# Performance work log

Hardware: AMD Instinct MI355X
Metric: run time of the kernel (lower is better)

Reference implementation:

```python
import jax, jax.numpy as jnp
import numpy as np

B, D_IN, D_H = 16384, 512, 1024


def _glorot(key, out_d, in_d):
    lim = 1.0 / np.sqrt(in_d)
    return jax.random.uniform(key, (out_d, in_d), minval=-lim, maxval=lim, dtype=jnp.float32)


def setup_inputs() -> dict:
    key = jax.random.key(0)
    ks = jax.random.split(key, 16)
    inp = {
        "x_t": jax.random.normal(ks[0], (B, D_IN), dtype=jnp.float32),
        "delta_t": jax.random.uniform(ks[1], (B, 1), dtype=jnp.float32),
        "h_prev": jax.random.normal(ks[2], (B, D_H), dtype=jnp.float32),
        # torch nn.Linear weights are [out, in]; y = x @ W.T
        "W_sh": _glorot(ks[3], D_H, D_H),
        "W_sx": _glorot(ks[4], D_H, D_IN),
        "W_st": _glorot(ks[5], D_H, 1),
        "b_s": jnp.zeros((D_H,), jnp.float32),
        "WTh": _glorot(ks[6], D_H, D_H),
        "WTx": _glorot(ks[7], D_H, D_IN),
        "WTs": _glorot(ks[8], D_H, D_H),
        "b_T": jnp.zeros((D_H,), jnp.float32),
        "W_rh": _glorot(ks[9], D_H, D_H),
        "W_rx": _glorot(ks[10], D_H, D_IN),
        "b_r": jnp.zeros((D_H,), jnp.float32),
        "W_zh": _glorot(ks[11], D_H, D_H),
        "W_zx": _glorot(ks[12], D_H, D_IN),
        "b_z": jnp.zeros((D_H,), jnp.float32),
        "W_h": _glorot(ks[13], D_H, D_H),
        "W_x": _glorot(ks[14], D_H, D_IN),
        "b": jnp.zeros((D_H,), jnp.float32),
    }
    return inp


def reference(x_t, delta_t, h_prev,
              W_sh, W_sx, W_st, b_s,
              WTh, WTx, WTs, b_T,
              W_rh, W_rx, b_r,
              W_zh, W_zx, b_z,
              W_h, W_x, b):
    lin = lambda x, W: x @ W.T  # nn.Linear(bias=False)
    s_t = jnp.tanh(lin(h_prev, W_sh) + lin(x_t, W_sx) + lin(delta_t, W_st) + b_s)
    T_t = jax.nn.sigmoid(lin(h_prev, WTh) + lin(x_t, WTx) + lin(s_t, WTs) + b_T)
    r_t = jax.nn.sigmoid(lin(h_prev, W_rh) + lin(x_t, W_rx) + b_r)
    z_t = jax.nn.sigmoid(lin(h_prev, W_zh) + lin(x_t, W_zx) + b_z)
    h_tilde = jnp.tanh(lin(r_t * h_prev, W_h) + lin(x_t, W_x) + b)
    h_t = (1.0 - z_t) * (T_t * h_prev) + z_t * h_tilde
    return h_t
```

## Files before the change

kernel.cpp:

```cpp
#include <hip/hip_runtime.h>
#include <stdint.h>

#define AS1 __attribute__((address_space(1)))
#define AS3 __attribute__((address_space(3)))

typedef unsigned short US;
typedef __bf16 bf16x8 __attribute__((ext_vector_type(8)));
typedef float f32x4 __attribute__((ext_vector_type(4)));
typedef int intx4 __attribute__((ext_vector_type(4)));

static constexpr int Bsz = 16384;
static constexpr int DIN = 512;
static constexpr int DH  = 1024;
static constexpr int LDA = 2560;
static constexpr int LDR = 1536;

__device__ __forceinline__ US f2bf(float f) {
  unsigned u = __float_as_uint(f);
  u += 0x7fffu + ((u >> 16) & 1u);
  return (US)(u >> 16);
}
__device__ __forceinline__ float bf2f(US u) { return __uint_as_float(((unsigned)u) << 16); }
__device__ __forceinline__ float sigm(float x) { return 1.f / (1.f + __expf(-x)); }
__device__ __forceinline__ float tanh_f(float x) { return 1.f - 2.f / (1.f + __expf(2.f * x)); }

__device__ __forceinline__ intx4 dsr128(unsigned addr) {
  intx4 r;
  asm volatile("ds_read_b128 %0, %1" : "=v"(r) : "v"(addr));
  return r;
}

#define BARR  __builtin_amdgcn_s_barrier()
#define SB0   __builtin_amdgcn_sched_barrier(0)
#define LGKM0 { asm volatile("s_waitcnt lgkmcnt(0)"); __builtin_amdgcn_sched_barrier(0); }
#define VMC8  { asm volatile("s_waitcnt vmcnt(8)"); __builtin_amdgcn_sched_barrier(0); }
#define VMC0  { asm volatile("s_waitcnt vmcnt(0)"); __builtin_amdgcn_sched_barrier(0); }

__global__ void pack_A(const float* __restrict__ h, const float* __restrict__ x,
                       US* __restrict__ Ab, US* __restrict__ RHx) {
  const int total = Bsz * 384;
  for (int idx = blockIdx.x * blockDim.x + threadIdx.x; idx < total;
       idx += gridDim.x * blockDim.x) {
    int row = idx / 384;
    int c = (idx - row * 384) * 4;
    const float* src = (c < DH) ? (h + (size_t)row * DH + c)
                                : (x + (size_t)row * DIN + (c - DH));
    float4 v = *(const float4*)src;
    ushort4 o;
    o.x = f2bf(v.x); o.y = f2bf(v.y); o.z = f2bf(v.z); o.w = f2bf(v.w);
    *(ushort4*)(Ab + (size_t)row * LDA + c) = o;
    if (c >= DH) *(ushort4*)(RHx + (size_t)row * LDR + c) = o;
  }
}

struct WSlot { const float* src; US* dst; int n4; int ksh; int ld; int co; };
struct WBatch { WSlot s[11]; };
__global__ void conv_w(WBatch b) {
  WSlot sl = b.s[blockIdx.y];
  const int mask = (1 << sl.ksh) - 1;
  for (int i = blockIdx.x * blockDim.x + threadIdx.x; i < sl.n4;
       i += gridDim.x * blockDim.x) {
    float4 v = *(const float4*)(sl.src + (size_t)i * 4);
    ushort4 o;
    o.x = f2bf(v.x); o.y = f2bf(v.y); o.z = f2bf(v.z); o.w = f2bf(v.w);
    int r = i >> sl.ksh;
    int cc = (i & mask) * 4;
    *(ushort4*)(sl.dst + (size_t)r * sl.ld + sl.co + cc) = o;
  }
}

template <int EPI, int NBLK>
__global__ __launch_bounds__(512, 2) void gemm8(
    const US* __restrict__ A, int lda,
    const US* __restrict__ W, int ldw, int nt,
    const float* __restrict__ bias0, const float* __restrict__ bias1,
    const float* __restrict__ bias2,
    const void* aux0, const void* aux1, const void* aux2,
    void* out0, int ldo0, void* out1, void* out2) {
  __shared__ __align__(16) US As[2][256 * 64];
  __shared__ __align__(16) US Bs[2][256 * 64];

  const int tid  = threadIdx.x;
  const int lane = tid & 63;
  const int w    = tid >> 6;
  const int wr   = w >> 2;
  const int wc   = w & 3;
  const int quad = lane >> 4, l15 = lane & 15;
  const int sw8  = l15 & 7;
  const int lrow = lane >> 3;
  const int scc  = (lane & 7) ^ (lrow & 7);

  const int p = blockIdx.x;
  const int c = p & 7, q = p >> 3;
  const int nIdx = q % NBLK, mIdx = c * 8 + q / NBLK;
  const int mBase = mIdx * 256, nBase = nIdx * 256;

  f32x4 acc[8][4];
#pragma unroll
  for (int i = 0; i < 8; i++)
#pragma unroll
    for (int j = 0; j < 4; j++) acc[i][j] = f32x4{0.f, 0.f, 0.f, 0.f};

  const unsigned aBase = (unsigned)(uintptr_t)&As[0][0];
  const unsigned bBase = (unsigned)(uintptr_t)&Bs[0][0];
  const unsigned arB = (unsigned)((wr * 128 + l15) * 128);
  const unsigned brB = (unsigned)((wc * 64 + l15) * 128);
  const unsigned kc0 = (unsigned)((quad ^ sw8) * 16);

  const size_t aRowS = (size_t)(mBase + w * 8 + lrow) * lda;
  const size_t wRowS = (size_t)(nBase + w * 8 + lrow) * ldw;
  const int sccOff = scc * 8;

#define STAGE_A(d, hh, co)                                                       \
  { const US* g = A + aRowS + (size_t)(hh) * 128 * lda + (co) + sccOff;          \
    __builtin_amdgcn_global_load_lds((AS1 const void*)g,                         \
        (AS3 void*)&As[d][((hh)*128 + w * 8) * 64], 16, 0, 0);                   \
    __builtin_amdgcn_global_load_lds((AS1 const void*)(g + (size_t)64 * lda),    \
        (AS3 void*)&As[d][((hh)*128 + 64 + w * 8) * 64], 16, 0, 0); }
#define STAGE_B(d, hh, co)                                                       \
  { const US* g = W + wRowS + (size_t)(hh) * 128 * ldw + (co) + sccOff;          \
    __builtin_amdgcn_global_load_lds((AS1 const void*)g,                         \
        (AS3 void*)&Bs[d][((hh)*128 + w * 8) * 64], 16, 0, 0);                   \
    __builtin_amdgcn_global_load_lds((AS1 const void*)(g + (size_t)64 * ldw),    \
        (AS3 void*)&Bs[d][((hh)*128 + 64 + w * 8) * 64], 16, 0, 0); }

#define READ_A(AF, mh)                                                           \
  _Pragma("unroll")                                                              \
  for (int i = 0; i < 4; ++i)                                                    \
    _Pragma("unroll")                                                            \
    for (int ks = 0; ks < 2; ++ks)                                               \
      AF[i][ks] = dsr128(aC + arB + (mh)*8192u + (unsigned)i * 2048u +           \
                         (kc0 ^ (unsigned)(ks << 6)));
#define READ_B(BSET, nh)                                                         \
  _Pragma("unroll")                                                              \
  for (int j = 0; j < 2; ++j)                                                    \
    _Pragma("unroll")                                                            \
    for (int ks = 0; ks < 2; ++ks)                                               \
      BSET[j][ks] = dsr128(bC + brB + (nh)*4096u + (unsigned)j * 2048u +         \
                           (kc0 ^ (unsigned)(ks << 6)));
#define MFMA_Q(AF, mh, BSET, nh)                                                 \
  _Pragma("unroll")                                                              \
  for (int ks = 0; ks < 2; ++ks)                                                 \
    _Pragma("unroll")                                                            \
    for (int i = 0; i < 4; ++i)                                                  \
      _Pragma("unroll")                                                          \
      for (int j = 0; j < 2; ++j)                                                \
        acc[(mh)*4 + i][(nh)*2 + j] = __builtin_amdgcn_mfma_f32_16x16x32_bf16(   \
            __builtin_bit_cast(bf16x8, AF[i][ks]),                               \
            __builtin_bit_cast(bf16x8, BSET[j][ks]),                             \
            acc[(mh)*4 + i][(nh)*2 + j], 0, 0, 0);

  STAGE_A(0, 0, 0); STAGE_A(0, 1, 0); STAGE_B(0, 0, 0); STAGE_B(0, 1, 0);
  STAGE_A(1, 0, 64); STAGE_A(1, 1, 64); STAGE_B(1, 0, 64); STAGE_B(1, 1, 64);
  VMC8;
  BARR;

  intx4 af0[4][2], af1[4][2], b0[2][2], b1[2][2];
  int cur = 0;

  for (int t = 0; t < nt; ++t, cur ^= 1) {
    const unsigned aC = aBase + (unsigned)cur * 32768u;
    const unsigned bC = bBase + (unsigned)cur * 32768u;
    const int co2 = (t + 2) * 64;
    READ_A(af0, 0);
    READ_A(af1, 1);
    READ_B(b0, 0);
    READ_B(b1, 1);
    LGKM0;
    BARR;
    if (t + 2 < nt) {
      STAGE_A(cur, 0, co2); STAGE_A(cur, 1, co2);
      STAGE_B(cur, 0, co2); STAGE_B(cur, 1, co2);
    }
    __builtin_amdgcn_s_setprio(1);
    MFMA_Q(af0, 0, b0, 0);
    MFMA_Q(af0, 0, b1, 1);
    MFMA_Q(af1, 1, b0, 0);
    MFMA_Q(af1, 1, b1, 1);
    __builtin_amdgcn_s_setprio(0);
    if (t + 1 < nt) {
      if (t + 2 < nt) { VMC8; } else { VMC0; }
      BARR;
    }
  }
#undef STAGE_A
#undef STAGE_B
#undef READ_A
#undef READ_B
#undef MFMA_Q

#pragma unroll
  for (int im = 0; im < 8; ++im) {
#pragma unroll
    for (int jn = 0; jn < 4; ++jn) {
      const int col = nBase + wc * 64 + jn * 16 + l15;
      if constexpr (EPI == 0) {
        const int g = nIdx >> 2;
        const int colg = col & 1023;
        const float* bp = (g == 0) ? bias0 : (g == 1) ? bias1 : bias2;
        const float bv = bp[colg];
        const float* delta = (const float*)aux0;
        const float* wst   = (const float*)aux1;
        const float* hp    = (const float*)aux2;
#pragma unroll
        for (int r = 0; r < 4; ++r) {
          const int row = mBase + wr * 128 + im * 16 + quad * 4 + r;
          float v = acc[im][jn][r] + bv;
          if (g == 0) {
            v += delta[row] * wst[colg];
            ((US*)out0)[(size_t)row * ldo0 + colg] = f2bf(tanh_f(v));
          } else if (g == 1) {
            float rr = sigm(v);
            ((US*)out1)[(size_t)row * LDR + colg] =
                f2bf(rr * hp[(size_t)row * DH + colg]);
          } else {
            ((US*)out2)[(size_t)row * DH + colg] = f2bf(sigm(v));
          }
        }
      } else if constexpr (EPI == 3) {
        const float bv = bias0[col];
#pragma unroll
        for (int r = 0; r < 4; ++r) {
          const int row = mBase + wr * 128 + im * 16 + quad * 4 + r;
          float v = acc[im][jn][r] + bv;
          ((US*)out0)[(size_t)row * ldo0 + col] = f2bf(tanh_f(v));
        }
      } else {
        const float bv = bias0[col];
        const float* hp = (const float*)aux0;
        const US* Zp = (const US*)aux1;
        const US* Hp = (const US*)aux2;
#pragma unroll
        for (int r = 0; r < 4; ++r) {
          const int row = mBase + wr * 128 + im * 16 + quad * 4 + r;
          float v = acc[im][jn][r] + bv;
          float T = sigm(v);
          size_t o = (size_t)row * DH + col;
          float z = bf2f(Zp[o]), ht = bf2f(Hp[o]);
          float h = hp[o];
          ((float*)out0)[(size_t)row * ldo0 + col] = (1.f - z) * (T * h) + z * ht;
        }
      }
    }
  }
}

extern "C" void kernel_launch(void* const* d_in, const int* in_sizes, int n_in,
                              void* d_out, int out_size, void* d_ws, size_t ws_size,
                              hipStream_t stream) {
  const float* x_t   = (const float*)d_in[0];
  const float* delta = (const float*)d_in[1];
  const float* h_prev= (const float*)d_in[2];
  const float* W_sh  = (const float*)d_in[3];
  const float* W_sx  = (const float*)d_in[4];
  const float* W_st  = (const float*)d_in[5];
  const float* b_s   = (const float*)d_in[6];
  const float* WTh   = (const float*)d_in[7];
  const float* WTx   = (const float*)d_in[8];
  const float* WTs   = (const float*)d_in[9];
  const float* b_T   = (const float*)d_in[10];
  const float* W_rh  = (const float*)d_in[11];
  const float* W_rx  = (const float*)d_in[12];
  const float* b_r   = (const float*)d_in[13];
  const float* W_zh  = (const float*)d_in[14];
  const float* W_zx  = (const float*)d_in[15];
  const float* b_z   = (const float*)d_in[16];
  const float* W_h   = (const float*)d_in[17];
  const float* W_x   = (const float*)d_in[18];
  const float* b_    = (const float*)d_in[19];
  float* out = (float*)d_out;

  char* ws = (char*)d_ws;
  US* Ab  = (US*)ws;              size_t off = (size_t)Bsz * LDA * 2;
  US* RH  = (US*)(ws + off);      off += (size_t)Bsz * LDR * 2;
  US* Zb  = (US*)(ws + off);      off += (size_t)Bsz * DH * 2;
  US* HTb = (US*)(ws + off);      off += (size_t)Bsz * DH * 2;
  US* bWsrz = (US*)(ws + off);    off += (size_t)3072 * 1536 * 2;
  US* bWT   = (US*)(ws + off);    off += (size_t)DH * 2560 * 2;
  US* bWh   = (US*)(ws + off);    off += (size_t)DH * 1536 * 2;

  pack_A<<<dim3(8192), 256, 0, stream>>>(h_prev, x_t, Ab, RH);
  WBatch wb;
  const int n4h = DH * DH / 4, n4x = DH * DIN / 4;
  US* bWr = bWsrz + (size_t)1024 * 1536;
  US* bWz = bWsrz + (size_t)2048 * 1536;
  wb.s[0]  = {W_sh, bWsrz, n4h, 8, 1536, 0};
  wb.s[1]  = {W_sx, bWsrz, n4x, 7, 1536, 1024};
  wb.s[2]  = {W_rh, bWr,   n4h, 8, 1536, 0};
  wb.s[3]  = {W_rx, bWr,   n4x, 7, 1536, 1024};
  wb.s[4]  = {W_zh, bWz,   n4h, 8, 1536, 0};
  wb.s[5]  = {W_zx, bWz,   n4x, 7, 1536, 1024};
  wb.s[6]  = {WTh,  bWT,   n4h, 8, 2560, 0};
  wb.s[7]  = {WTx,  bWT,   n4x, 7, 2560, 1024};
  wb.s[8]  = {WTs,  bWT,   n4h, 8, 2560, 1536};
  wb.s[9]  = {W_h,  bWh,   n4h, 8, 1536, 0};
  wb.s[10] = {W_x,  bWh,   n4x, 7, 1536, 1024};
  conv_w<<<dim3(512, 11), 256, 0, stream>>>(wb);

  gemm8<0, 12><<<dim3(768), 512, 0, stream>>>(
      Ab, LDA, bWsrz, 1536, 24, b_s, b_r, b_z,
      delta, W_st, h_prev, (void*)(Ab + 1536), LDA, (void*)RH, (void*)Zb);
  gemm8<3, 4><<<dim3(256), 512, 0, stream>>>(
      RH, LDR, bWh, 1536, 24, b_, nullptr, nullptr,
      nullptr, nullptr, nullptr, (void*)HTb, DH, nullptr, nullptr);
  gemm8<4, 4><<<dim3(256), 512, 0, stream>>>(
      Ab, LDA, bWT, 2560, 40, b_T, nullptr, nullptr,
      h_prev, Zb, HTb, (void*)out, DH, nullptr, nullptr);
}
```

Baseline: 672.5 us.

## Interleave LDS reads and global staging across four MFMA quadrants per k-step

Restructures the GEMM main loop into a finer-grained ping-pong schedule. LDS fragment reads and global-to-LDS staging of the A/B halves are now spread between the four MFMA quadrants. One A half-tile is staged one iteration ahead instead of two, and the vmcnt wait drops from 8 to 6. The intent is to overlap memory traffic with MFMA work and cut the long stall before compute. The cost is many more barriers per iteration and tighter dependency timing.

```diff
diff --git a/kernel.cpp b/kernel.cpp
--- a/kernel.cpp
+++ b/kernel.cpp
@@ -33,7 +33,7 @@
 #define BARR  __builtin_amdgcn_s_barrier()
 #define SB0   __builtin_amdgcn_sched_barrier(0)
 #define LGKM0 { asm volatile("s_waitcnt lgkmcnt(0)"); __builtin_amdgcn_sched_barrier(0); }
-#define VMC8  { asm volatile("s_waitcnt vmcnt(8)"); __builtin_amdgcn_sched_barrier(0); }
+#define VMC6  { asm volatile("s_waitcnt vmcnt(6)"); __builtin_amdgcn_sched_barrier(0); }
 #define VMC0  { asm volatile("s_waitcnt vmcnt(0)"); __builtin_amdgcn_sched_barrier(0); }
 
 __global__ void pack_A(const float* __restrict__ h, const float* __restrict__ x,
@@ -151,8 +151,8 @@
             acc[(mh)*4 + i][(nh)*2 + j], 0, 0, 0);
 
   STAGE_A(0, 0, 0); STAGE_A(0, 1, 0); STAGE_B(0, 0, 0); STAGE_B(0, 1, 0);
-  STAGE_A(1, 0, 64); STAGE_A(1, 1, 64); STAGE_B(1, 0, 64); STAGE_B(1, 1, 64);
-  VMC8;
+  STAGE_B(1, 0, 64); STAGE_B(1, 1, 64); STAGE_A(1, 0, 64);
+  VMC6;
   BARR;
 
   intx4 af0[4][2], af1[4][2], b0[2][2], b1[2][2];
@@ -161,25 +161,40 @@
   for (int t = 0; t < nt; ++t, cur ^= 1) {
     const unsigned aC = aBase + (unsigned)cur * 32768u;
     const unsigned bC = bBase + (unsigned)cur * 32768u;
-    const int co2 = (t + 2) * 64;
+    const int nxt = cur ^ 1;
+    const bool s1 = (t + 1 < nt), s2 = (t + 2 < nt);
+    const int co1 = (t + 1) * 64, co2 = (t + 2) * 64;
     READ_A(af0, 0);
-    READ_A(af1, 1);
     READ_B(b0, 0);
-    READ_B(b1, 1);
+    if (s1) STAGE_A(nxt, 1, co1);
+    BARR;
     LGKM0;
-    BARR;
-    if (t + 2 < nt) {
-      STAGE_A(cur, 0, co2); STAGE_A(cur, 1, co2);
-      STAGE_B(cur, 0, co2); STAGE_B(cur, 1, co2);
-    }
     __builtin_amdgcn_s_setprio(1);
     MFMA_Q(af0, 0, b0, 0);
+    __builtin_amdgcn_s_setprio(0);
+    BARR;
+    READ_B(b1, 1);
+    BARR;
+    LGKM0;
+    __builtin_amdgcn_s_setprio(1);
     MFMA_Q(af0, 0, b1, 1);
+    __builtin_amdgcn_s_setprio(0);
+    BARR;
+    READ_A(af1, 1);
+    if (s2) STAGE_B(cur, 0, co2);
+    BARR;
+    LGKM0;
+    __builtin_amdgcn_s_setprio(1);
     MFMA_Q(af1, 1, b0, 0);
+    __builtin_amdgcn_s_setprio(0);
+    BARR;
+    if (s2) { STAGE_B(cur, 1, co2); STAGE_A(cur, 0, co2); }
+    BARR;
+    __builtin_amdgcn_s_setprio(1);
     MFMA_Q(af1, 1, b1, 1);
     __builtin_amdgcn_s_setprio(0);
-    if (t + 1 < nt) {
-      if (t + 2 < nt) { VMC8; } else { VMC0; }
+    if (s1) {
+      if (s2) { VMC6; } else { VMC0; }
       BARR;
     }
   }
```

After: 678.9 us. About the same (+1.0%).
